# Optimization experiments

Measured on AMD Instinct MI355X. Metric: run time of the kernel, lower is better.

Reference implementation:

```python
import math
import jax, jax.numpy as jnp
import numpy as np

CAPACITY_FACTOR = 1.0
LOAD_BALANCE_RATIO = 0.01


def setup_inputs() -> dict:
    key = jax.random.key(0)
    k1, k2 = jax.random.split(key)
    x = jax.random.normal(k1, (16384, 4096), dtype=jnp.float32)
    wg = jax.random.normal(k2, (4096, 64), dtype=jnp.float32) * 0.02
    return {"x": x, "wg": wg}


def reference(x, wg):
    # router logits: [S, E]
    logits = jnp.einsum('sd,de->se', x, wg)
    gates = jax.nn.softmax(logits, axis=1)
    S, E = gates.shape
    capacity_fp = max(min(float(S), S / E * CAPACITY_FACTOR), 4.0)
    capacity = math.ceil(capacity_fp)

    # top-1 expert per token
    indices_s = jnp.argmax(gates, axis=1)                  # [S] int
    mask1 = jax.nn.one_hot(indices_s, E, dtype=jnp.int32)  # [S, E]

    # load-balance statistics
    me = jnp.sum(gates, axis=0) / S                        # router prob fraction
    ce = jnp.sum(mask1.astype(jnp.float32), axis=0) / S    # dispatch fraction

    # position of each token within its expert queue
    locations1 = jnp.cumsum(mask1, axis=0) - 1             # [S, E]
    # 'cut' token drop: keep only tokens within capacity
    mask1 = mask1 * (locations1 < capacity).astype(jnp.int32)
    locations1_s = jnp.sum(locations1 * mask1, axis=1)     # [S]
    mask_sum = jnp.sum(mask1, axis=1)                      # [S]

    # dispatch mask: [E, capacity] of token ids (-1 = empty slot)
    token_ids = jnp.arange(S, dtype=jnp.int32)
    dispatch_indices = jnp.where(mask_sum == 0, -1, indices_s * capacity + locations1_s)
    dispatch_mask = jnp.full((E * capacity + 1,), -1, dtype=jnp.int32)
    dispatch_mask = dispatch_mask.at[dispatch_indices].set(token_ids)
    dispatch_mask = dispatch_mask[:-1].reshape(E, capacity)

    # combine weight per token (0 for dropped tokens)
    gates1_s = jnp.sum(gates * mask1.astype(jnp.float32), axis=1).reshape(1, -1)

    # load-balance aux loss (Switch/GShard form) * ratio
    loss = LOAD_BALANCE_RATIO * E * jnp.sum(me * ce)
    return loss, gates1_s, dispatch_mask
```

## Files before the change

kernel.cpp:

```cpp
#include <hip/hip_runtime.h>
#include <math.h>

#define S_TOK 16384
#define DDIM  4096
#define NEXP  64
#define CAP   256
#define NB    256
#define TM    256
#define KT    32
#define SPLITS 8
#define KRANGE (DDIM / SPLITS)
#define NTILE (KRANGE / KT)
#define MT    (S_TOK / TM)
#define APAD  260

template <int ATOMIC>
__global__ __launch_bounds__(256, 2) void gemm_split_kernel(
    const float* __restrict__ x, const float* __restrict__ wg,
    float* __restrict__ outbuf)
{
    __shared__ float AT[KT * APAD];
    __shared__ float Bs[KT * NEXP];

    const int t   = threadIdx.x;
    const int ty  = t >> 3;
    const int tx  = t & 7;
    const int blk = blockIdx.x;
    const int m   = blk & (MT - 1);
    const int s   = blk >> 6;
    const int mBase = m * TM;
    const int kBase = s * KRANGE;

    float acc[8][8] = {};
    float4 av[8], bv0, bv1;

    auto loadRegs = [&](int tile) {
        const int k0 = kBase + tile * KT;
#pragma unroll
        for (int p = 0; p < 8; p++) {
            int flat = p * 256 + t;
            int tok = flat >> 3, kf = flat & 7;
            av[p] = *reinterpret_cast<const float4*>(
                &x[(size_t)(mBase + tok) * DDIM + k0 + kf * 4]);
        }
        int fl0 = t, fl1 = 256 + t;
        bv0 = *reinterpret_cast<const float4*>(
            &wg[(size_t)(k0 + (fl0 >> 4)) * NEXP + (fl0 & 15) * 4]);
        bv1 = *reinterpret_cast<const float4*>(
            &wg[(size_t)(k0 + (fl1 >> 4)) * NEXP + (fl1 & 15) * 4]);
    };

    loadRegs(0);
    for (int tile = 0; tile < NTILE; tile++) {
        __syncthreads();
#pragma unroll
        for (int p = 0; p < 8; p++) {
            int flat = p * 256 + t;
            int tok = flat >> 3, kf = flat & 7;
#pragma unroll
            for (int j = 0; j < 4; j++)
                AT[(kf * 4 + j) * APAD + tok] = (&av[p].x)[j];
        }
        {
            int fl0 = t, fl1 = 256 + t;
            *reinterpret_cast<float4*>(&Bs[(fl0 >> 4) * NEXP + (fl0 & 15) * 4]) = bv0;
            *reinterpret_cast<float4*>(&Bs[(fl1 >> 4) * NEXP + (fl1 & 15) * 4]) = bv1;
        }
        __syncthreads();
        if (tile + 1 < NTILE) loadRegs(tile + 1);
#pragma unroll
        for (int k = 0; k < KT; k++) {
            float4 a0 = *reinterpret_cast<const float4*>(&AT[k * APAD + ty * 8]);
            float4 a1 = *reinterpret_cast<const float4*>(&AT[k * APAD + ty * 8 + 4]);
            float4 b0 = *reinterpret_cast<const float4*>(&Bs[k * NEXP + tx * 8]);
            float4 b1 = *reinterpret_cast<const float4*>(&Bs[k * NEXP + tx * 8 + 4]);
            float aa[8] = {a0.x, a0.y, a0.z, a0.w, a1.x, a1.y, a1.z, a1.w};
            float bb[8] = {b0.x, b0.y, b0.z, b0.w, b1.x, b1.y, b1.z, b1.w};
#pragma unroll
            for (int i = 0; i < 8; i++)
#pragma unroll
                for (int j = 0; j < 8; j++)
                    acc[i][j] = fmaf(aa[i], bb[j], acc[i][j]);
        }
    }

#pragma unroll
    for (int i = 0; i < 8; i++) {
        size_t row = (size_t)(mBase + ty * 8 + i) * NEXP + tx * 8;
        if (ATOMIC) {
#pragma unroll
            for (int j = 0; j < 8; j++) atomicAdd(&outbuf[row + j], acc[i][j]);
        } else {
            float* dst = outbuf + (size_t)s * (S_TOK * NEXP) + row;
            *reinterpret_cast<float4*>(dst) =
                make_float4(acc[i][0], acc[i][1], acc[i][2], acc[i][3]);
            *reinterpret_cast<float4*>(dst + 4) =
                make_float4(acc[i][4], acc[i][5], acc[i][6], acc[i][7]);
        }
    }
}

__global__ __launch_bounds__(256) void softmax_kernel(
    const float* __restrict__ buf, int nsplits,
    int* __restrict__ arg_idx, float* __restrict__ gateval,
    int* __restrict__ cnt_part, float* __restrict__ gsum_blk)
{
    __shared__ int   cnt_sh[4][NEXP];
    __shared__ float gs_sh[NEXP];
    const int t = threadIdx.x;
    const int w = t >> 6, lane = t & 63;
    const int tok = blockIdx.x * 256 + t;

    if (t < NEXP) gs_sh[t] = 0.f;
    cnt_sh[w][lane] = 0;
    __syncthreads();

    float4 r[16];
    {
        const float* p = buf + (size_t)tok * NEXP;
#pragma unroll
        for (int q = 0; q < 16; q++)
            r[q] = *reinterpret_cast<const float4*>(p + q * 4);
    }
    for (int sp = 1; sp < nsplits; sp++) {
        const float* ps = buf + (size_t)sp * (S_TOK * NEXP) + (size_t)tok * NEXP;
#pragma unroll
        for (int q = 0; q < 16; q++) {
            float4 v = *reinterpret_cast<const float4*>(ps + q * 4);
            r[q].x += v.x; r[q].y += v.y; r[q].z += v.z; r[q].w += v.w;
        }
    }

    float m_ = r[0].x; int b_ = 0;
#pragma unroll
    for (int q = 0; q < 16; q++)
#pragma unroll
        for (int j = 0; j < 4; j++) {
            float v = (&r[q].x)[j];
            int e = q * 4 + j;
            if (v > m_) { m_ = v; b_ = e; }
        }

    float den = 0.f;
#pragma unroll
    for (int q = 0; q < 16; q++)
#pragma unroll
        for (int j = 0; j < 4; j++) {
            float g = __expf((&r[q].x)[j] - m_);
            (&r[q].x)[j] = g;
            den += g;
        }
    float inv = 1.f / den;

    arg_idx[tok] = b_;
    gateval[tok] = inv;
    atomicAdd(&cnt_sh[w][b_], 1);

#pragma unroll
    for (int q = 0; q < 16; q++)
#pragma unroll
        for (int j = 0; j < 4; j++) {
            float v = (&r[q].x)[j] * inv;
#pragma unroll
            for (int msk = 1; msk < 64; msk <<= 1) v += __shfl_xor(v, msk, 64);
            if (lane == 0) atomicAdd(&gs_sh[q * 4 + j], v);
        }

    __syncthreads();
    cnt_part[(blockIdx.x * 4 + w) * NEXP + lane] = cnt_sh[w][lane];
    if (t < NEXP) gsum_blk[blockIdx.x * NEXP + t] = gs_sh[t];
}

__global__ __launch_bounds__(256) void scan_kernel(
    const int* __restrict__ cnt_part, const float* __restrict__ gsum_blk,
    int* __restrict__ offsets, float* __restrict__ loss_out)
{
    __shared__ int qs[4][NEXP];
    const int t = threadIdx.x;
    const int e = t & 63, q = t >> 6;

    int s = 0;
    for (int i = 0; i < 64; i++) s += cnt_part[(q * 64 + i) * NEXP + e];
    qs[q][e] = s;
    __syncthreads();

    int base = 0;
    for (int q2 = 0; q2 < q; q2++) base += qs[q2][e];
    int run = base;
    for (int i = 0; i < 64; i++) {
        int b = q * 64 + i;
        offsets[b * NEXP + e] = run;
        run += cnt_part[b * NEXP + e];
    }

    if (q == 0) {
        float totg = 0.f;
        for (int i = 0; i < 64; i++) totg += gsum_blk[i * NEXP + e];
        int totc = qs[0][e] + qs[1][e] + qs[2][e] + qs[3][e];
        float lp = (totg / (float)S_TOK) * ((float)totc / (float)S_TOK);
#pragma unroll
        for (int msk = 1; msk < 64; msk <<= 1) lp += __shfl_xor(lp, msk, 64);
        if (t == 0) loss_out[0] = 0.01f * (float)NEXP * lp;
    }
}

__global__ __launch_bounds__(64) void dispatch_kernel(
    const int* __restrict__ arg_idx, const float* __restrict__ gateval,
    const int* __restrict__ offsets,
    float* __restrict__ out_gates, float* __restrict__ out_disp)
{
    __shared__ int sh_e[64];
    const int t = threadIdx.x, blk = blockIdx.x;
    const int tok = blk * 64 + t;
    const int e = arg_idx[tok];
    sh_e[t] = e;
    __syncthreads();
    int rank = 0;
    for (int j = 0; j < t; j++) rank += (sh_e[j] == e);
    int loc = offsets[blk * NEXP + e] + rank;
    float gv = 0.f;
    if (loc < CAP) {
        gv = gateval[tok];
        out_disp[e * CAP + loc] = (float)tok;
    }
    out_gates[tok] = gv;
}

__global__ __launch_bounds__(256) void init_disp_kernel(float* __restrict__ p)
{
    p[blockIdx.x * 256 + threadIdx.x] = -1.0f;
}

__global__ __launch_bounds__(256) void zero_kernel(float* __restrict__ p, int n4)
{
    int i = blockIdx.x * 256 + threadIdx.x;
    float4 z = make_float4(0.f, 0.f, 0.f, 0.f);
    for (; i < n4; i += gridDim.x * 256)
        reinterpret_cast<float4*>(p)[i] = z;
}

extern "C" void kernel_launch(void* const* d_in, const int* in_sizes, int n_in,
                              void* d_out, int out_size, void* d_ws, size_t ws_size,
                              hipStream_t stream)
{
    const float* x  = (const float*)d_in[0];
    const float* wg = (const float*)d_in[1];

    float* out       = (float*)d_out;
    float* out_loss  = out;
    float* out_gates = out + 1;
    float* out_disp  = out + 1 + S_TOK;

    char* ws = (char*)d_ws;
    int*   arg_idx  = (int*)(ws);
    float* gateval  = (float*)(ws + (64 << 10));
    int*   cnt_part = (int*)(ws + (128 << 10));
    float* gsum_blk = (float*)(ws + (192 << 10));
    int*   offsets  = (int*)(ws + (208 << 10));
    float* buf      = (float*)(ws + (512 << 10));

    const size_t splitBytes = (size_t)SPLITS * S_TOK * NEXP * sizeof(float);
    const bool use_split = ws_size >= (512u << 10) + splitBytes;

    hipLaunchKernelGGL(init_disp_kernel, dim3(NEXP * CAP / 256), dim3(256), 0,
                       stream, out_disp);

    if (use_split) {
        hipLaunchKernelGGL((gemm_split_kernel<0>), dim3(MT * SPLITS), dim3(256),
                           0, stream, x, wg, buf);
        hipLaunchKernelGGL(softmax_kernel, dim3(S_TOK / 256), dim3(256), 0,
                           stream, buf, SPLITS, arg_idx, gateval, cnt_part,
                           gsum_blk);
    } else {
        hipLaunchKernelGGL(zero_kernel, dim3(256), dim3(256), 0, stream,
                           buf, S_TOK * NEXP / 4);
        hipLaunchKernelGGL((gemm_split_kernel<1>), dim3(MT * SPLITS), dim3(256),
                           0, stream, x, wg, buf);
        hipLaunchKernelGGL(softmax_kernel, dim3(S_TOK / 256), dim3(256), 0,
                           stream, buf, 1, arg_idx, gateval, cnt_part,
                           gsum_blk);
    }

    hipLaunchKernelGGL(scan_kernel, dim3(1), dim3(256), 0, stream,
                       cnt_part, gsum_blk, offsets, out_loss);
    hipLaunchKernelGGL(dispatch_kernel, dim3(NB), dim3(64), 0, stream,
                       arg_idx, gateval, offsets, out_gates, out_disp);
}
```

Measured before the change: 593.3 us.

## Restructure router GEMM to one token per thread with async LDS loads

```diff
diff --git a/kernel.cpp b/kernel.cpp
--- a/kernel.cpp
+++ b/kernel.cpp
@@ -6,97 +6,86 @@
 #define NEXP  64
 #define CAP   256
 #define NB    256
-#define TM    256
-#define KT    32
 #define SPLITS 8
 #define KRANGE (DDIM / SPLITS)
+#define KT    32
 #define NTILE (KRANGE / KT)
-#define MT    (S_TOK / TM)
-#define APAD  260
+#define MTILES (S_TOK / 64)
+
+__device__ __forceinline__ void gload_lds16(const float* g, float* l)
+{
+    __builtin_amdgcn_global_load_lds(
+        (const __attribute__((address_space(1))) void*)g,
+        (__attribute__((address_space(3))) void*)l, 16, 0, 0);
+}
 
 template <int ATOMIC>
-__global__ __launch_bounds__(256, 2) void gemm_split_kernel(
+__global__ __launch_bounds__(64, 4) void gemm_tok_kernel(
     const float* __restrict__ x, const float* __restrict__ wg,
     float* __restrict__ outbuf)
 {
-    __shared__ float AT[KT * APAD];
-    __shared__ float Bs[KT * NEXP];
+    __shared__ float AT[2][KT * 64];
 
     const int t   = threadIdx.x;
-    const int ty  = t >> 3;
-    const int tx  = t & 7;
     const int blk = blockIdx.x;
-    const int m   = blk & (MT - 1);
-    const int s   = blk >> 6;
-    const int mBase = m * TM;
+    const int m   = blk & (MTILES - 1);
+    const int s   = blk >> 8;
+    const int mBase = m * 64;
     const int kBase = s * KRANGE;
 
-    float acc[8][8] = {};
-    float4 av[8], bv0, bv1;
-
-    auto loadRegs = [&](int tile) {
+    float acc[NEXP] = {};
+
+    auto stage = [&](int buf, int tile) {
         const int k0 = kBase + tile * KT;
 #pragma unroll
-        for (int p = 0; p < 8; p++) {
-            int flat = p * 256 + t;
-            int tok = flat >> 3, kf = flat & 7;
-            av[p] = *reinterpret_cast<const float4*>(
-                &x[(size_t)(mBase + tok) * DDIM + k0 + kf * 4]);
-        }
-        int fl0 = t, fl1 = 256 + t;
-        bv0 = *reinterpret_cast<const float4*>(
-            &wg[(size_t)(k0 + (fl0 >> 4)) * NEXP + (fl0 & 15) * 4]);
-        bv1 = *reinterpret_cast<const float4*>(
-            &wg[(size_t)(k0 + (fl1 >> 4)) * NEXP + (fl1 & 15) * 4]);
+        for (int c = 0; c < 8; c++) {
+            int P   = c * 64 + t;
+            int tok = P >> 3;
+            int kc  = (P & 7) ^ (tok & 7);
+            gload_lds16(&x[(size_t)(mBase + tok) * DDIM + k0 + kc * 4],
+                        &AT[buf][P * 4]);
+        }
     };
 
-    loadRegs(0);
+    stage(0, 0);
     for (int tile = 0; tile < NTILE; tile++) {
+        asm volatile("s_waitcnt vmcnt(0)" ::: "memory");
         __syncthreads();
-#pragma unroll
-        for (int p = 0; p < 8; p++) {
-            int flat = p * 256 + t;
-            int tok = flat >> 3, kf = flat & 7;
-#pragma unroll
-            for (int j = 0; j < 4; j++)
-                AT[(kf * 4 + j) * APAD + tok] = (&av[p].x)[j];
-        }
-        {
-            int fl0 = t, fl1 = 256 + t;
-            *reinterpret_cast<float4*>(&Bs[(fl0 >> 4) * NEXP + (fl0 & 15) * 4]) = bv0;
-            *reinterpret_cast<float4*>(&Bs[(fl1 >> 4) * NEXP + (fl1 & 15) * 4]) = bv1;
-        }
-        __syncthreads();
-        if (tile + 1 < NTILE) loadRegs(tile + 1);
-#pragma unroll
-        for (int k = 0; k < KT; k++) {
-            float4 a0 = *reinterpret_cast<const float4*>(&AT[k * APAD + ty * 8]);
-            float4 a1 = *reinterpret_cast<const float4*>(&AT[k * APAD + ty * 8 + 4]);
-            float4 b0 = *reinterpret_cast<const float4*>(&Bs[k * NEXP + tx * 8]);
-            float4 b1 = *reinterpret_cast<const float4*>(&Bs[k * NEXP + tx * 8 + 4]);
-            float aa[8] = {a0.x, a0.y, a0.z, a0.w, a1.x, a1.y, a1.z, a1.w};
-            float bb[8] = {b0.x, b0.y, b0.z, b0.w, b1.x, b1.y, b1.z, b1.w};
-#pragma unroll
-            for (int i = 0; i < 8; i++)
-#pragma unroll
-                for (int j = 0; j < 8; j++)
-                    acc[i][j] = fmaf(aa[i], bb[j], acc[i][j]);
-        }
-    }
-
-#pragma unroll
-    for (int i = 0; i < 8; i++) {
-        size_t row = (size_t)(mBase + ty * 8 + i) * NEXP + tx * 8;
-        if (ATOMIC) {
-#pragma unroll
-            for (int j = 0; j < 8; j++) atomicAdd(&outbuf[row + j], acc[i][j]);
-        } else {
-            float* dst = outbuf + (size_t)s * (S_TOK * NEXP) + row;
-            *reinterpret_cast<float4*>(dst) =
-                make_float4(acc[i][0], acc[i][1], acc[i][2], acc[i][3]);
-            *reinterpret_cast<float4*>(dst + 4) =
-                make_float4(acc[i][4], acc[i][5], acc[i][6], acc[i][7]);
-        }
+        if (tile + 1 < NTILE) stage((tile + 1) & 1, tile + 1);
+        const int k0 = kBase + tile * KT;
+        const float* At = AT[tile & 1];
+#pragma unroll
+        for (int kc = 0; kc < 8; kc++) {
+            float4 a4 = *reinterpret_cast<const float4*>(
+                &At[(t * 8 + (kc ^ (t & 7))) * 4]);
+#pragma unroll
+            for (int j = 0; j < 4; j++) {
+                const float a = (&a4.x)[j];
+                const float4* bk = reinterpret_cast<const float4*>(
+                    &wg[(size_t)(k0 + kc * 4 + j) * NEXP]);
+#pragma unroll
+                for (int e4 = 0; e4 < 16; e4++) {
+                    float4 b = bk[e4];
+                    acc[e4 * 4 + 0] = fmaf(a, b.x, acc[e4 * 4 + 0]);
+                    acc[e4 * 4 + 1] = fmaf(a, b.y, acc[e4 * 4 + 1]);
+                    acc[e4 * 4 + 2] = fmaf(a, b.z, acc[e4 * 4 + 2]);
+                    acc[e4 * 4 + 3] = fmaf(a, b.w, acc[e4 * 4 + 3]);
+                }
+            }
+        }
+    }
+
+    const size_t row = (size_t)(mBase + t) * NEXP;
+    if (ATOMIC) {
+#pragma unroll
+        for (int e = 0; e < NEXP; e++) atomicAdd(&outbuf[row + e], acc[e]);
+    } else {
+        float* dst = outbuf + (size_t)s * ((size_t)S_TOK * NEXP) + row;
+#pragma unroll
+        for (int e4 = 0; e4 < 16; e4++)
+            reinterpret_cast<float4*>(dst)[e4] =
+                make_float4(acc[e4 * 4 + 0], acc[e4 * 4 + 1],
+                            acc[e4 * 4 + 2], acc[e4 * 4 + 3]);
     }
 }
 
@@ -123,7 +112,8 @@
             r[q] = *reinterpret_cast<const float4*>(p + q * 4);
     }
     for (int sp = 1; sp < nsplits; sp++) {
-        const float* ps = buf + (size_t)sp * (S_TOK * NEXP) + (size_t)tok * NEXP;
+        const float* ps = buf + (size_t)sp * ((size_t)S_TOK * NEXP)
+                              + (size_t)tok * NEXP;
 #pragma unroll
         for (int q = 0; q < 16; q++) {
             float4 v = *reinterpret_cast<const float4*>(ps + q * 4);
@@ -266,7 +256,7 @@
                        stream, out_disp);
 
     if (use_split) {
-        hipLaunchKernelGGL((gemm_split_kernel<0>), dim3(MT * SPLITS), dim3(256),
+        hipLaunchKernelGGL((gemm_tok_kernel<0>), dim3(MTILES * SPLITS), dim3(64),
                            0, stream, x, wg, buf);
         hipLaunchKernelGGL(softmax_kernel, dim3(S_TOK / 256), dim3(256), 0,
                            stream, buf, SPLITS, arg_idx, gateval, cnt_part,
@@ -274,7 +264,7 @@
     } else {
         hipLaunchKernelGGL(zero_kernel, dim3(256), dim3(256), 0, stream,
                            buf, S_TOK * NEXP / 4);
-        hipLaunchKernelGGL((gemm_split_kernel<1>), dim3(MT * SPLITS), dim3(256),
+        hipLaunchKernelGGL((gemm_tok_kernel<1>), dim3(MTILES * SPLITS), dim3(64),
                            0, stream, x, wg, buf);
         hipLaunchKernelGGL(softmax_kernel, dim3(S_TOK / 256), dim3(256), 0,
                            stream, buf, 1, arg_idx, gateval, cnt_part,
```

New measurement: 727.4 us. 22.6% more time.
